# Kernel tuning notes

Measured on AMD Instinct MI355X. Metric: run time of the kernel, lower is better.

Reference implementation:

```python
import jax, jax.numpy as jnp
import numpy as np
from jax import lax

D = 384      # embd_d
L = 4        # num_blocks
B = 64
SHW, THW = 24, 12
NS, NT = SHW * SHW, THW * THW   # 576, 144
EPS = 1e-5


def _ln(x, g, b):
    mu = jnp.mean(x, axis=-1, keepdims=True)
    var = jnp.mean(jnp.square(x - mu), axis=-1, keepdims=True)
    return (x - mu) * lax.rsqrt(var + EPS) * g + b


def setup_inputs() -> dict:
    key = jax.random.key(0)
    ks = iter(jax.random.split(key, 64))
    f32 = jnp.float32
    def nrm(shape, s=0.02):
        return jax.random.normal(next(ks), shape, dtype=f32) * s
    inp = {
        'search': jax.random.normal(next(ks), (B, NS, D), dtype=f32),
        'target': jax.random.normal(next(ks), (B, NT, D), dtype=f32),
        # learned tokens / positional params
        'cls': nrm((1, 1, D), 1.0),
        'search_pos': nrm((1, NS, D), 0.5),
        'target_pos': nrm((1, NT, D), 0.5),
        # stacked per-block params [L, ...]
        'ln1_g': jnp.ones((L, D), f32), 'ln1_b': jnp.zeros((L, D), f32),
        'Wq': nrm((L, D, D)), 'bq': jnp.zeros((L, D), f32),
        'Wk': nrm((L, D, D)), 'bk': jnp.zeros((L, D), f32),
        'Wv': nrm((L, D, D)), 'bv': jnp.zeros((L, D), f32),
        'ln2_g': jnp.ones((L, D), f32), 'ln2_b': jnp.zeros((L, D), f32),
        'W1': nrm((L, D, 2 * D)), 'b1': jnp.zeros((L, 2 * D), f32),
        'W2': nrm((L, 2 * D, D)), 'b2': jnp.zeros((L, D), f32),
        # head
        'lnf_g': jnp.ones((D,), f32), 'lnf_b': jnp.zeros((D,), f32),
        'Wl1': nrm((D, D)), 'bl1': jnp.zeros((D,), f32),
        'Wl2': nrm((D, 1)), 'bl2': jnp.zeros((1,), f32),
    }
    return inp


def reference(search, target, cls, search_pos, target_pos,
              ln1_g, ln1_b, Wq, bq, Wk, bk, Wv, bv,
              ln2_g, ln2_b, W1, b1, W2, b2,
              lnf_g, lnf_b, Wl1, bl1, Wl2, bl2):
    scale = D ** (-0.5)  # note: full embed dim, as in source
    x = jnp.concatenate([
        jnp.broadcast_to(cls, (B, 1, D)),
        search + search_pos,
        target + target_pos,
    ], axis=1)  # [B, 1+Ns+Nt, D]

    def block(x, p):
        l1g, l1b, wq, bq_, wk, bk_, wv, bv_, l2g, l2b, w1, b1_, w2, b2_ = p
        y = _ln(x, l1g, l1b)
        q = y @ wq + bq_
        k = y @ wk + bk_
        v = y @ wv + bv_
        attn = jax.nn.softmax(jnp.einsum('bid,bjd->bij', q, k) * scale, axis=-1)
        x = x + jnp.einsum('bij,bjd->bid', attn, v)
        h = _ln(x, l2g, l2b)
        x = x + (jax.nn.gelu(h @ w1 + b1_, approximate=False) @ w2 + b2_)
        return x, None

    x, _ = lax.scan(block, x, (ln1_g, ln1_b, Wq, bq, Wk, bk, Wv, bv,
                               ln2_g, ln2_b, W1, b1, W2, b2))
    h = _ln(x[:, 0], lnf_g, lnf_b)          # cls token [B, D]
    h = jax.nn.relu(h @ Wl1 + bl1)
    return h @ Wl2 + bl2                     # [B, 1]
```

## Files before the change

kernel.cpp:

```cpp
#include <hip/hip_runtime.h>
#include <hip/hip_bf16.h>
#include <math.h>

#define DD 384
#define NBATCH 64
#define NSEQ 721
#define NROWS (NBATCH*NSEQ)
#define NLAYER 4
#define VTW 736

typedef __bf16 bf16_t;
typedef __bf16 bf16x8 __attribute__((ext_vector_type(8)));
typedef float  f32x4  __attribute__((ext_vector_type(4)));

static __device__ __forceinline__ void split_bf16(float v, bf16_t& h, bf16_t& l) {
    h = (bf16_t)v;
    l = (bf16_t)(v - (float)h);
}
static __device__ __forceinline__ bf16x8 bzero8() {
    bf16x8 v = {(bf16_t)0.f,(bf16_t)0.f,(bf16_t)0.f,(bf16_t)0.f,
                (bf16_t)0.f,(bf16_t)0.f,(bf16_t)0.f,(bf16_t)0.f};
    return v;
}
static __device__ __forceinline__ void gload16(const void* g, void* l) {
    __builtin_amdgcn_global_load_lds(
        (const __attribute__((address_space(1))) unsigned int*)g,
        (__attribute__((address_space(3))) unsigned int*)l, 16, 0, 0);
}
static __device__ __forceinline__ int xcd_swz(int nwg) {
    int orig = blockIdx.x;
    int q = nwg >> 3, r = nwg & 7;
    int xcd = orig & 7, within = orig >> 3;
    int base = (xcd < r) ? xcd*(q+1) : r*(q+1) + (xcd - r)*q;
    return base + within;
}
static __device__ __forceinline__ void ln_from_partials(const float* ss, const float* ss2,
                                                        int row, float& mu, float& rstd) {
    float s = 0.f, q2 = 0.f;
    #pragma unroll
    for (int k = 0; k < 6; ++k) { s += ss[k*NROWS + row]; q2 += ss2[k*NROWS + row]; }
    mu = s * (1.f/DD);
    float var = q2 * (1.f/DD) - mu*mu;
    rstd = rsqrtf(var + 1e-5f);
}

__global__ __launch_bounds__(256) void build_x_kernel(const float* __restrict__ search,
                               const float* __restrict__ target,
                               const float* __restrict__ cls,
                               const float* __restrict__ spos,
                               const float* __restrict__ tpos,
                               bf16_t* __restrict__ xh, bf16_t* __restrict__ xl,
                               float* __restrict__ wss, float* __restrict__ wss2) {
    int wave = threadIdx.x >> 6, lane = threadIdx.x & 63;
    int row = blockIdx.x * 4 + wave;
    if (row >= NROWS) return;
    int b = row / NSEQ, n = row % NSEQ;
    float s = 0.f, q2 = 0.f;
    #pragma unroll
    for (int i = 0; i < 6; ++i) {
        int d = lane + 64*i;
        float val;
        if (n == 0)        val = cls[d];
        else if (n <= 576) val = search[((size_t)b*576 + (n-1))*DD + d] + spos[(size_t)(n-1)*DD + d];
        else               val = target[((size_t)b*144 + (n-577))*DD + d] + tpos[(size_t)(n-577)*DD + d];
        bf16_t h, l;
        split_bf16(val, h, l);
        xh[(size_t)row*DD + d] = h;
        xl[(size_t)row*DD + d] = l;
        s += val; q2 += val*val;
    }
    #pragma unroll
    for (int m = 1; m < 64; m <<= 1) { s += __shfl_xor(s, m); q2 += __shfl_xor(q2, m); }
    if (lane == 0) {
        wss[row] = s; wss2[row] = q2;
        #pragma unroll
        for (int k = 1; k < 6; ++k) { wss[k*NROWS + row] = 0.f; wss2[k*NROWS + row] = 0.f; }
    }
}

__global__ void transpose_split_kernel(const float* __restrict__ src,
                                       const float* __restrict__ g,
                                       bf16_t* __restrict__ dh,
                                       bf16_t* __restrict__ dl,
                                       int K, int N) {
    int idx = blockIdx.x * blockDim.x + threadIdx.x;
    if (idx >= K*N) return;
    int k = idx / N, n = idx % N;
    float v = src[idx];
    if (g) v *= g[k];
    bf16_t h, l;
    split_bf16(v, h, l);
    dh[(size_t)n*K + k] = h;
    dl[(size_t)n*K + k] = l;
}

__global__ void colsum_kernel(const float* __restrict__ W, const float* __restrict__ g,
                              const float* __restrict__ b, const float* __restrict__ bias,
                              float* __restrict__ c1, float* __restrict__ c2,
                              int K, int N, int outStride, int outOff) {
    int l = blockIdx.y;
    int n = blockIdx.x * 256 + threadIdx.x;
    if (n >= N) return;
    const float* Wl = W + (size_t)l*K*N;
    const float* gl = g + (size_t)l*K;
    const float* bl = b + (size_t)l*K;
    float s1 = 0.f, s2 = 0.f;
    for (int k = 0; k < K; ++k) {
        float w = Wl[(size_t)k*N + n];
        s1 = fmaf(gl[k], w, s1);
        s2 = fmaf(bl[k], w, s2);
    }
    c1[(size_t)l*outStride + outOff + n] = s1;
    c2[(size_t)l*outStride + outOff + n] = s2 + bias[(size_t)l*N + n];
}

static __device__ __forceinline__ void gemm_core(
        const bf16_t* __restrict__ ah, const bf16_t* __restrict__ al,
        const bf16_t* __restrict__ bh, const bf16_t* __restrict__ bl,
        bf16_t (&ls)[32][64][8],
        int m0, int n0, int K, f32x4 (&acc)[4][4]) {
    int t = threadIdx.x;
    int w = t >> 6, lane = t & 63;
    int c = lane & 15, g = lane >> 4;
    int wr = w >> 1, wc = w & 1;
    const bf16_t* src0 = (w==0) ? ah : (w==1) ? al : (w==2) ? bh : bl;
    int base_rc = (w < 2) ? m0 : n0;
    const bf16_t* srcbase = src0 + (size_t)(base_rc + c)*K + 8*g;

    int ksteps = K >> 5;
    for (int kt = 0; kt < ksteps; ++kt) {
        int k0 = kt << 5;
        __syncthreads();
        #pragma unroll
        for (int i = 0; i < 8; ++i)
            gload16(srcbase + (size_t)(16*i)*K + k0, &ls[w*8 + i][0][0]);
        __syncthreads();
        bf16x8 af_h[4], af_l[4], bf_h[4], bf_l[4];
        #pragma unroll
        for (int i = 0; i < 4; ++i) {
            af_h[i] = *(const bf16x8*)&ls[     4*wr + i][lane][0];
            af_l[i] = *(const bf16x8*)&ls[ 8 + 4*wr + i][lane][0];
            bf_h[i] = *(const bf16x8*)&ls[16 + 4*wc + i][lane][0];
            bf_l[i] = *(const bf16x8*)&ls[24 + 4*wc + i][lane][0];
        }
        #pragma unroll
        for (int i = 0; i < 4; ++i)
            #pragma unroll
            for (int j = 0; j < 4; ++j) {
                acc[i][j] = __builtin_amdgcn_mfma_f32_16x16x32_bf16(af_h[i], bf_h[j], acc[i][j], 0,0,0);
                acc[i][j] = __builtin_amdgcn_mfma_f32_16x16x32_bf16(af_h[i], bf_l[j], acc[i][j], 0,0,0);
                acc[i][j] = __builtin_amdgcn_mfma_f32_16x16x32_bf16(af_l[i], bf_h[j], acc[i][j], 0,0,0);
            }
    }
}

__global__ __launch_bounds__(256, 4) void gemm_qkv(
        const bf16_t* __restrict__ ah, const bf16_t* __restrict__ al,
        const bf16_t* __restrict__ bh, const bf16_t* __restrict__ bl,
        const float* __restrict__ ss, const float* __restrict__ ss2,
        const float* __restrict__ c1, const float* __restrict__ c2,
        bf16_t* __restrict__ qout, bf16_t* __restrict__ kout,
        bf16_t* __restrict__ vth, bf16_t* __restrict__ vtl,
        int nwg) {
    __shared__ __align__(16) bf16_t ls[32][64][8];
    int wgid = xcd_swz(nwg);
    int mt = wgid / 9, n0 = (wgid % 9) * 128;
    int blb = mt / 6;
    int tok_base = (mt % 6) * 128;
    int m0d = blb*NSEQ + tok_base;
    f32x4 zero4 = {0.f,0.f,0.f,0.f};
    f32x4 acc[4][4];
    #pragma unroll
    for (int i = 0; i < 4; ++i)
        #pragma unroll
        for (int j = 0; j < 4; ++j) acc[i][j] = zero4;
    gemm_core(ah, al, bh, bl, ls, m0d, n0, DD, acc);

    int t = threadIdx.x, w = t >> 6, lane = t & 63;
    int c = lane & 15, g = lane >> 4;
    int wr = w >> 1, wc = w & 1;
    float rmu[16], rrs[16];
    #pragma unroll
    for (int i = 0; i < 4; ++i)
        #pragma unroll
        for (int r = 0; r < 4; ++r) {
            int tok = tok_base + 64*wr + 16*i + 4*g + r;
            float mu = 0.f, rstd = 1.f;
            if (tok < NSEQ) ln_from_partials(ss, ss2, blb*NSEQ + tok, mu, rstd);
            rmu[i*4+r] = mu; rrs[i*4+r] = rstd;
        }
    int seg = n0 / 384;
    if (seg < 2) {
        bf16_t* outb = (seg == 0) ? qout : kout;
        int segoff = seg * 384;
        #pragma unroll
        for (int j = 0; j < 4; ++j) {
            int nglob = n0 + 64*wc + 16*j + c;
            int nloc = nglob - segoff;
            float C1 = c1[nglob], C2 = c2[nglob];
            #pragma unroll
            for (int i = 0; i < 4; ++i) {
                #pragma unroll
                for (int r = 0; r < 4; ++r) {
                    int tok = tok_base + 64*wr + 16*i + 4*g + r;
                    if (tok >= NSEQ) continue;
                    float val = rrs[i*4+r]*(acc[i][j][r] - rmu[i*4+r]*C1) + C2;
                    outb[(size_t)(blb*NSEQ + tok)*DD + nloc] = (bf16_t)val;
                }
            }
        }
    } else {
        int vbase = n0 - 768;
        bf16_t* LST = &ls[0][0][0];
        #pragma unroll
        for (int pass = 0; pass < 2; ++pass) {
            __syncthreads();
            #pragma unroll
            for (int j = 0; j < 4; ++j) {
                int d = 64*wc + 16*j + c;
                float C1 = c1[n0 + 64*wc + 16*j + c];
                float C2 = c2[n0 + 64*wc + 16*j + c];
                #pragma unroll
                for (int i = 0; i < 4; ++i)
                    #pragma unroll
                    for (int r = 0; r < 4; ++r) {
                        int tokl = 64*wr + 16*i + 4*g + r;
                        float val = rrs[i*4+r]*(acc[i][j][r] - rmu[i*4+r]*C1) + C2;
                        if (tok_base + tokl >= NSEQ) val = 0.f;
                        bf16_t h, l;
                        split_bf16(val, h, l);
                        LST[d*128 + (tokl ^ ((d & 15) << 3))] = pass ? l : h;
                    }
            }
            __syncthreads();
            bf16_t* outp = pass ? vtl : vth;
            #pragma unroll
            for (int p = 0; p < 8; ++p) {
                int chunk = t + 256*p;
                int d = chunk >> 4;
                int tok0 = (chunk & 15) * 8;
                int tg = tok_base + tok0;
                if (tg + 8 > VTW) continue;
                uint4 v = *(const uint4*)&LST[d*128 + (tok0 ^ ((d & 15) << 3))];
                *(uint4*)(outp + ((size_t)(blb*DD + vbase + d))*VTW + tg) = v;
            }
        }
    }
}

template<int EPI, int NT>
__global__ __launch_bounds__(256, 4) void gemm_mfma(
        const bf16_t* __restrict__ ah, const bf16_t* __restrict__ al,
        const bf16_t* __restrict__ bh, const bf16_t* __restrict__ bl,
        const float* __restrict__ ss, const float* __restrict__ ss2,
        const float* __restrict__ c1, const float* __restrict__ c2,
        const float* __restrict__ bias,
        const bf16_t* __restrict__ resh, const bf16_t* __restrict__ resl,
        bf16_t* __restrict__ o1, bf16_t* __restrict__ o2,
        float* __restrict__ wss, float* __restrict__ wss2,
        int M, int N, int K, int nwg) {
    __shared__ __align__(16) bf16_t ls[32][64][8];
    int wgid = xcd_swz(nwg);
    int m0 = (wgid / NT) * 128, n0 = (wgid % NT) * 128;
    f32x4 zero4 = {0.f,0.f,0.f,0.f};
    f32x4 acc[4][4];
    #pragma unroll
    for (int i = 0; i < 4; ++i)
        #pragma unroll
        for (int j = 0; j < 4; ++j) acc[i][j] = zero4;
    gemm_core(ah, al, bh, bl, ls, m0, n0, K, acc);

    int t = threadIdx.x, w = t >> 6, lane = t & 63;
    int c = lane & 15, g = lane >> 4;
    int wr = w >> 1, wc = w & 1;

    if (EPI == 2) {
        float rmu[16], rrs[16];
        #pragma unroll
        for (int i = 0; i < 4; ++i)
            #pragma unroll
            for (int r = 0; r < 4; ++r) {
                int row = m0 + 64*wr + 16*i + 4*g + r;
                float mu = 0.f, rstd = 1.f;
                if (row < M) ln_from_partials(ss, ss2, row, mu, rstd);
                rmu[i*4+r] = mu; rrs[i*4+r] = rstd;
            }
        #pragma unroll
        for (int j = 0; j < 4; ++j) {
            int n = n0 + 64*wc + 16*j + c;
            float C1 = c1[n], C2 = c2[n];
            #pragma unroll
            for (int i = 0; i < 4; ++i) {
                int rbase = m0 + 64*wr + 16*i + 4*g;
                #pragma unroll
                for (int r = 0; r < 4; ++r) {
                    int row = rbase + r;
                    if (row >= M) continue;
                    float val = rrs[i*4+r]*(acc[i][j][r] - rmu[i*4+r]*C1) + C2;
                    val = 0.5f*val*(1.0f + erff(val*0.70710678118654752f));
                    bf16_t h, l;
                    split_bf16(val, h, l);
                    size_t o = (size_t)row*N + n;
                    o1[o] = h;
                    o2[o] = l;
                }
            }
        }
    } else {
        int slot = (wgid % NT) + 3*wc;
        #pragma unroll
        for (int i = 0; i < 4; ++i)
            #pragma unroll
            for (int r = 0; r < 4; ++r) {
                int row = m0 + 64*wr + 16*i + 4*g + r;
                if (row >= M) continue;
                float s = 0.f, q2 = 0.f;
                #pragma unroll
                for (int j = 0; j < 4; ++j) {
                    int n = n0 + 64*wc + 16*j + c;
                    size_t o = (size_t)row*N + n;
                    float val = acc[i][j][r] + bias[n] + (float)resh[o] + (float)resl[o];
                    bf16_t h, l;
                    split_bf16(val, h, l);
                    o1[o] = h;
                    o2[o] = l;
                    s += val; q2 += val*val;
                }
                #pragma unroll
                for (int m = 1; m < 16; m <<= 1) { s += __shfl_xor(s, m); q2 += __shfl_xor(q2, m); }
                if (c == 0) {
                    wss[slot*NROWS + row] = s;
                    wss2[slot*NROWS + row] = q2;
                }
            }
    }
}

__global__ __launch_bounds__(256, 2) void attn_mfma(
        const bf16_t* __restrict__ qh, const bf16_t* __restrict__ kh,
        const bf16_t* __restrict__ vth, const bf16_t* __restrict__ vtl,
        bf16_t* __restrict__ xh, bf16_t* __restrict__ xl,
        float* __restrict__ wss, float* __restrict__ wss2, int nwg) {
    __shared__ __align__(16) char smem[73728];
    bf16_t* kf = (bf16_t*)smem;
    char* vhp = smem + 24576;
    char* vlp = smem + 49152;

    int t = threadIdx.x, w = t >> 6, lane = t & 63;
    int c = lane & 15, g = lane >> 4;
    int wgid = xcd_swz(nwg);
    int bl_ = wgid / 12;
    int q0 = (wgid % 12) * 64;
    size_t bb = (size_t)bl_ * NSEQ;
    int qrow = q0 + 16*w + c;
    bool qok = (qrow < NSEQ);
    const float scale = 0.05103103630798287f;
    int vswz = (c ^ (c >> 2)) & 3;
    int dma_dd  = lane >> 2;
    int dma_kv8 = (lane & 3) ^ ((dma_dd ^ (dma_dd >> 2)) & 3);

    bf16x8 qf[12];
    #pragma unroll
    for (int ks = 0; ks < 12; ++ks) {
        if (qok) qf[ks] = *(const bf16x8*)(qh + (bb + qrow)*DD + 32*ks + 8*g);
        else     qf[ks] = bzero8();
    }

    f32x4 zero4 = {0.f,0.f,0.f,0.f};
    f32x4 oacc[24];
    #pragma unroll
    for (int i = 0; i < 24; ++i) oacc[i] = zero4;
    float m_run = -1e30f, l_run = 0.f;

    #pragma unroll
    for (int i = 0; i < 6; ++i) {
        int s = i*4 + w;
        int ks = s >> 1, mf = s & 1;
        gload16(kh + (bb + (size_t)(16*mf + c))*DD + 32*ks + 8*g, kf + s*512);
    }

    for (int kt = 0; kt < 23; ++kt) {
        int kv0 = kt * 32;
        asm volatile("s_waitcnt vmcnt(0)" ::: "memory");
        __builtin_amdgcn_s_barrier();
        #pragma unroll
        for (int i = 0; i < 6; ++i) {
            int s = i*4 + w;
            size_t gro = ((size_t)(bl_*DD + 16*s + dma_dd))*VTW + kv0 + 8*dma_kv8;
            gload16(vth + gro, (bf16_t*)vhp + s*512);
            gload16(vtl + gro, (bf16_t*)vlp + s*512);
        }
        f32x4 sacc[2];
        sacc[0] = zero4; sacc[1] = zero4;
        #pragma unroll
        for (int ks = 0; ks < 12; ++ks) {
            bf16x8 a0 = *(const bf16x8*)(kf + ((size_t)(2*ks+0)*64 + lane)*8);
            bf16x8 a1 = *(const bf16x8*)(kf + ((size_t)(2*ks+1)*64 + lane)*8);
            sacc[0] = __builtin_amdgcn_mfma_f32_16x16x32_bf16(a0, qf[ks], sacc[0], 0,0,0);
            sacc[1] = __builtin_amdgcn_mfma_f32_16x16x32_bf16(a1, qf[ks], sacc[1], 0,0,0);
        }
        float p[2][4];
        float mx = -1e30f;
        #pragma unroll
        for (int mf = 0; mf < 2; ++mf)
            #pragma unroll
            for (int r = 0; r < 4; ++r) {
                float sv = sacc[mf][r] * scale;
                int kv = kv0 + 16*mf + 4*g + r;
                if (kv >= NSEQ) sv = -1e30f;
                p[mf][r] = sv;
                mx = fmaxf(mx, sv);
            }
        mx = fmaxf(mx, __shfl_xor(mx, 16));
        mx = fmaxf(mx, __shfl_xor(mx, 32));
        float m_new = fmaxf(m_run, mx);
        float corr = __expf(m_run - m_new);
        float psum = 0.f;
        #pragma unroll
        for (int mf = 0; mf < 2; ++mf)
            #pragma unroll
            for (int r = 0; r < 4; ++r) {
                float pv = __expf(p[mf][r] - m_new);
                p[mf][r] = pv;
                psum += pv;
            }
        psum += __shfl_xor(psum, 16);
        psum += __shfl_xor(psum, 32);
        l_run = l_run * corr + psum;
        m_run = m_new;
        #pragma unroll
        for (int i = 0; i < 24; ++i) oacc[i] *= corr;
        bf16x8 ph, pl;
        #pragma unroll
        for (int mf = 0; mf < 2; ++mf)
            #pragma unroll
            for (int r = 0; r < 4; ++r) {
                bf16_t hh, ll;
                split_bf16(p[mf][r], hh, ll);
                ph[mf*4 + r] = hh;
                pl[mf*4 + r] = ll;
            }
        asm volatile("s_waitcnt vmcnt(0)" ::: "memory");
        __builtin_amdgcn_s_barrier();
        if (kt + 1 < 23) {
            int kv0n = kv0 + 32;
            #pragma unroll
            for (int i = 0; i < 6; ++i) {
                int s = i*4 + w;
                int ks = s >> 1, mf = s & 1;
                gload16(kh + (bb + (size_t)(kv0n + 16*mf + c))*DD + 32*ks + 8*g, kf + s*512);
            }
        }
        #pragma unroll
        for (int mf = 0; mf < 24; ++mf) {
            int dr = 16*mf + c;
            const char* vb  = vhp + dr*64;
            const char* vb2 = vlp + dr*64;
            int o0 = ((((g>>1)     ^ vswz) << 4) | (8*(g&1)));
            int o1 = (((2 + (g>>1)) ^ vswz) << 4) | (8*(g&1));
            union { uint2 u[2]; bf16x8 v; } va, vc2;
            va.u[0]  = *(const uint2*)(vb  + o0);
            va.u[1]  = *(const uint2*)(vb  + o1);
            vc2.u[0] = *(const uint2*)(vb2 + o0);
            vc2.u[1] = *(const uint2*)(vb2 + o1);
            oacc[mf] = __builtin_amdgcn_mfma_f32_16x16x32_bf16(va.v,  ph, oacc[mf], 0,0,0);
            oacc[mf] = __builtin_amdgcn_mfma_f32_16x16x32_bf16(va.v,  pl, oacc[mf], 0,0,0);
            oacc[mf] = __builtin_amdgcn_mfma_f32_16x16x32_bf16(vc2.v, ph, oacc[mf], 0,0,0);
        }
    }
    float inv = 1.f / l_run;
    float s = 0.f, q2 = 0.f;
    if (qok) {
        bf16_t* xhr = xh + (bb + qrow)*DD;
        bf16_t* xlr = xl + (bb + qrow)*DD;
        #pragma unroll
        for (int mf = 0; mf < 24; ++mf)
            #pragma unroll
            for (int r = 0; r < 4; ++r) {
                int d = 16*mf + 4*g + r;
                float xv = (float)xhr[d] + (float)xlr[d] + oacc[mf][r]*inv;
                bf16_t h, l;
                split_bf16(xv, h, l);
                xhr[d] = h;
                xlr[d] = l;
                s += xv; q2 += xv*xv;
            }
    }
    s += __shfl_xor(s, 16);  q2 += __shfl_xor(q2, 16);
    s += __shfl_xor(s, 32);  q2 += __shfl_xor(q2, 32);
    if (qok && g == 0) {
        int rowL = bl_*NSEQ + qrow;
        wss[rowL] = s; wss2[rowL] = q2;
        #pragma unroll
        for (int k = 1; k < 6; ++k) { wss[k*NROWS + rowL] = 0.f; wss2[k*NROWS + rowL] = 0.f; }
    }
}

__global__ __launch_bounds__(384) void head_kernel(const bf16_t* __restrict__ xh,
    const bf16_t* __restrict__ xl,
    const float* __restrict__ g, const float* __restrict__ bb,
    const float* __restrict__ Wl1, const float* __restrict__ bl1,
    const float* __restrict__ Wl2, const float* __restrict__ bl2,
    float* __restrict__ outp) {
    __shared__ float yv[384];
    __shared__ float r1[6], r2[6], r3[6];
    int b = blockIdx.x, t = threadIdx.x;
    size_t o = (size_t)b*NSEQ*DD + t;
    float v = (float)xh[o] + (float)xl[o];
    float s = v;
    #pragma unroll
    for (int m = 1; m < 64; m <<= 1) s += __shfl_xor(s, m);
    if ((t & 63) == 0) r1[t>>6] = s;
    __syncthreads();
    float mu = (r1[0]+r1[1]+r1[2]+r1[3]+r1[4]+r1[5]) * (1.f/384.f);
    float dd = v - mu;
    float sq = dd*dd;
    #pragma unroll
    for (int m = 1; m < 64; m <<= 1) sq += __shfl_xor(sq, m);
    if ((t & 63) == 0) r2[t>>6] = sq;
    __syncthreads();
    float var = (r2[0]+r2[1]+r2[2]+r2[3]+r2[4]+r2[5]) * (1.f/384.f);
    float rstd = rsqrtf(var + 1e-5f);
    yv[t] = dd*rstd*g[t] + bb[t];
    __syncthreads();
    float acc = bl1[t];
    for (int d2 = 0; d2 < 384; d2++) acc = fmaf(yv[d2], Wl1[d2*384 + t], acc);
    acc = fmaxf(acc, 0.f);
    float oo = acc * Wl2[t];
    #pragma unroll
    for (int m = 1; m < 64; m <<= 1) oo += __shfl_xor(oo, m);
    if ((t & 63) == 0) r3[t>>6] = oo;
    __syncthreads();
    if (t == 0) outp[b] = r3[0]+r3[1]+r3[2]+r3[3]+r3[4]+r3[5] + bl2[0];
}

extern "C" void kernel_launch(void* const* d_in, const int* in_sizes, int n_in,
                              void* d_out, int out_size, void* d_ws, size_t ws_size,
                              hipStream_t stream) {
    const float* search = (const float*)d_in[0];
    const float* target = (const float*)d_in[1];
    const float* cls    = (const float*)d_in[2];
    const float* spos   = (const float*)d_in[3];
    const float* tpos   = (const float*)d_in[4];
    const float* ln1_g  = (const float*)d_in[5];
    const float* ln1_b  = (const float*)d_in[6];
    const float* Wq     = (const float*)d_in[7];
    const float* bq     = (const float*)d_in[8];
    const float* Wk     = (const float*)d_in[9];
    const float* bk     = (const float*)d_in[10];
    const float* Wv     = (const float*)d_in[11];
    const float* bv     = (const float*)d_in[12];
    const float* ln2_g  = (const float*)d_in[13];
    const float* ln2_b  = (const float*)d_in[14];
    const float* W1     = (const float*)d_in[15];
    const float* b1     = (const float*)d_in[16];
    const float* W2     = (const float*)d_in[17];
    const float* b2     = (const float*)d_in[18];
    const float* lnf_g  = (const float*)d_in[19];
    const float* lnf_b  = (const float*)d_in[20];
    const float* Wl1    = (const float*)d_in[21];
    const float* bl1    = (const float*)d_in[22];
    const float* Wl2    = (const float*)d_in[23];
    const float* bl2    = (const float*)d_in[24];

    size_t off = 0;
    char* base = (char*)d_ws;
    auto alloc = [&](size_t bytes) -> void* {
        void* p = base + off;
        off += (bytes + 255) & ~(size_t)255;
        return p;
    };

    bf16_t* xh = (bf16_t*)alloc((size_t)NROWS * DD * 2);
    bf16_t* xl = (bf16_t*)alloc((size_t)NROWS * DD * 2);
    float* ssum  = (float*)alloc((size_t)6*NROWS*4);
    float* ssum2 = (float*)alloc((size_t)6*NROWS*4);

    const int SQKV = 1152*DD;
    const int SM = DD*768;
    bf16_t* wqkvh = (bf16_t*)alloc((size_t)4*SQKV*2);
    bf16_t* wqkvl = (bf16_t*)alloc((size_t)4*SQKV*2);
    bf16_t* w1h = (bf16_t*)alloc((size_t)4*SM*2);
    bf16_t* w1l = (bf16_t*)alloc((size_t)4*SM*2);
    bf16_t* w2h = (bf16_t*)alloc((size_t)4*SM*2);
    bf16_t* w2l = (bf16_t*)alloc((size_t)4*SM*2);
    float* cqkv1 = (float*)alloc((size_t)4*1152*4);
    float* cqkv2 = (float*)alloc((size_t)4*1152*4);
    float* cm11  = (float*)alloc((size_t)4*768*4);
    float* cm12  = (float*)alloc((size_t)4*768*4);

    const size_t qB  = (size_t)NSEQ*DD*2;
    const size_t vB  = (size_t)DD*VTW*2;
    const size_t mB  = (size_t)NSEQ*768*2;
    const size_t perB = 2*qB + 2*vB;
    size_t avail = (ws_size > off + 262144) ? (ws_size - off - 262144) : 0;
    int G = (int)(avail / perB);
    if (G > NBATCH) G = NBATCH;
    if (G < 1) G = 1;

    char* U = (char*)alloc(perB * G);
    bf16_t* qhB  = (bf16_t*)U;
    bf16_t* khB  = (bf16_t*)(U + qB*G);
    bf16_t* vth  = (bf16_t*)(U + 2*qB*G);
    bf16_t* vtl  = (bf16_t*)(U + 2*qB*G + vB*G);
    bf16_t* midh = (bf16_t*)U;
    bf16_t* midl = (bf16_t*)(U + mB*G);

    build_x_kernel<<<(NROWS+3)/4, 256, 0, stream>>>(search, target, cls, spos, tpos,
                                                    xh, xl, ssum, ssum2);

    const int SQ = DD*DD;
    for (int l = 0; l < NLAYER; ++l) {
        bf16_t* dsth = wqkvh + (size_t)l*SQKV;
        bf16_t* dstl = wqkvl + (size_t)l*SQKV;
        transpose_split_kernel<<<(SQ+255)/256, 256, 0, stream>>>(Wq + (size_t)l*SQ, ln1_g + l*DD, dsth,          dstl,          DD, DD);
        transpose_split_kernel<<<(SQ+255)/256, 256, 0, stream>>>(Wk + (size_t)l*SQ, ln1_g + l*DD, dsth + 384*DD, dstl + 384*DD, DD, DD);
        transpose_split_kernel<<<(SQ+255)/256, 256, 0, stream>>>(Wv + (size_t)l*SQ, ln1_g + l*DD, dsth + 768*DD, dstl + 768*DD, DD, DD);
        transpose_split_kernel<<<(SM+255)/256, 256, 0, stream>>>(W1 + (size_t)l*SM, ln2_g + l*DD, w1h + (size_t)l*SM, w1l + (size_t)l*SM, DD, 768);
        transpose_split_kernel<<<(SM+255)/256, 256, 0, stream>>>(W2 + (size_t)l*SM, nullptr,      w2h + (size_t)l*SM, w2l + (size_t)l*SM, 768, DD);
    }
    colsum_kernel<<<dim3(2, NLAYER), 256, 0, stream>>>(Wq, ln1_g, ln1_b, bq, cqkv1, cqkv2, DD, DD, 1152, 0);
    colsum_kernel<<<dim3(2, NLAYER), 256, 0, stream>>>(Wk, ln1_g, ln1_b, bk, cqkv1, cqkv2, DD, DD, 1152, 384);
    colsum_kernel<<<dim3(2, NLAYER), 256, 0, stream>>>(Wv, ln1_g, ln1_b, bv, cqkv1, cqkv2, DD, DD, 1152, 768);
    colsum_kernel<<<dim3(3, NLAYER), 256, 0, stream>>>(W1, ln2_g, ln2_b, b1, cm11, cm12, DD, 768, 768, 0);

    for (int l = 0; l < NLAYER; ++l) {
        for (int b0 = 0; b0 < NBATCH; b0 += G) {
            int cb = (NBATCH - b0 < G) ? (NBATCH - b0) : G;
            int Mc = cb * NSEQ;
            bf16_t* xch = xh + (size_t)b0 * NSEQ * DD;
            bf16_t* xcl = xl + (size_t)b0 * NSEQ * DD;
            float* ssc  = ssum  + (size_t)b0 * NSEQ;
            float* ssc2 = ssum2 + (size_t)b0 * NSEQ;
            int mtiles = (Mc + 127)/128;
            int nwgQKV = 9*6*cb, nwgM1 = 6*mtiles, nwgM2 = 3*mtiles, nwgA = 12*cb;

            gemm_qkv<<<nwgQKV, 256, 0, stream>>>(xch, xcl,
                    wqkvh + (size_t)l*SQKV, wqkvl + (size_t)l*SQKV,
                    ssc, ssc2, cqkv1 + l*1152, cqkv2 + l*1152,
                    qhB, khB, vth, vtl, nwgQKV);
            attn_mfma<<<nwgA, 256, 0, stream>>>(qhB, khB, vth, vtl, xch, xcl,
                    ssc, ssc2, nwgA);
            gemm_mfma<2,6><<<nwgM1, 256, 0, stream>>>(xch, xcl,
                    w1h + (size_t)l*SM, w1l + (size_t)l*SM,
                    ssc, ssc2, cm11 + l*768, cm12 + l*768, nullptr,
                    nullptr, nullptr, midh, midl, nullptr, nullptr, Mc, 768, DD, nwgM1);
            gemm_mfma<3,3><<<nwgM2, 256, 0, stream>>>(midh, midl,
                    w2h + (size_t)l*SM, w2l + (size_t)l*SM,
                    nullptr, nullptr, nullptr, nullptr, b2 + l*DD,
                    xch, xcl, xch, xcl, ssc, ssc2, Mc, DD, 768, nwgM2);
        }
    }
    head_kernel<<<NBATCH, 384, 0, stream>>>(xh, xl, lnf_g, lnf_b, Wl1, bl1, Wl2, bl2, (float*)d_out);
}
```

Before: 3.596 ms.

## Drop V low-precision split, stage Q/K stores through LDS, add lazy softmax rescale

Removes the bf16 hi/lo split for V, so attention loads only one V buffer and issues two MFMAs per tile instead of three. This halves V traffic and LDS use, which allows three workgroups per CU. Q/K outputs are now staged through LDS for coalesced 16-byte stores. The online softmax skips the max update and accumulator rescale when the new max stays within a threshold of the running max. The workspace sizing now uses the MLP intermediate size. The cost is lower precision in the attention-times-V product.

```diff
diff --git a/kernel.cpp b/kernel.cpp
--- a/kernel.cpp
+++ b/kernel.cpp
@@ -160,7 +160,7 @@
         const float* __restrict__ ss, const float* __restrict__ ss2,
         const float* __restrict__ c1, const float* __restrict__ c2,
         bf16_t* __restrict__ qout, bf16_t* __restrict__ kout,
-        bf16_t* __restrict__ vth, bf16_t* __restrict__ vtl,
+        bf16_t* __restrict__ vth,
         int nwg) {
     __shared__ __align__(16) bf16_t ls[32][64][8];
     int wgid = xcd_swz(nwg);
@@ -190,60 +190,62 @@
             rmu[i*4+r] = mu; rrs[i*4+r] = rstd;
         }
     int seg = n0 / 384;
+    bf16_t* LST = &ls[0][0][0];
     if (seg < 2) {
         bf16_t* outb = (seg == 0) ? qout : kout;
         int segoff = seg * 384;
+        __syncthreads();
         #pragma unroll
         for (int j = 0; j < 4; ++j) {
-            int nglob = n0 + 64*wc + 16*j + c;
-            int nloc = nglob - segoff;
-            float C1 = c1[nglob], C2 = c2[nglob];
-            #pragma unroll
-            for (int i = 0; i < 4; ++i) {
+            int nl = 64*wc + 16*j + c;
+            float C1 = c1[n0 + nl], C2 = c2[n0 + nl];
+            #pragma unroll
+            for (int i = 0; i < 4; ++i)
                 #pragma unroll
                 for (int r = 0; r < 4; ++r) {
-                    int tok = tok_base + 64*wr + 16*i + 4*g + r;
-                    if (tok >= NSEQ) continue;
+                    int rl = 64*wr + 16*i + 4*g + r;
                     float val = rrs[i*4+r]*(acc[i][j][r] - rmu[i*4+r]*C1) + C2;
-                    outb[(size_t)(blb*NSEQ + tok)*DD + nloc] = (bf16_t)val;
+                    LST[rl*128 + (nl ^ ((rl & 15) << 3))] = (bf16_t)val;
                 }
-            }
+        }
+        __syncthreads();
+        #pragma unroll
+        for (int p = 0; p < 8; ++p) {
+            int chunk = t + 256*p;
+            int rl = chunk >> 4;
+            int nl0 = (chunk & 15) * 8;
+            int tok = tok_base + rl;
+            if (tok >= NSEQ) continue;
+            uint4 v = *(const uint4*)&LST[rl*128 + (nl0 ^ ((rl & 15) << 3))];
+            *(uint4*)(outb + (size_t)(blb*NSEQ + tok)*DD + (n0 - segoff) + nl0) = v;
         }
     } else {
         int vbase = n0 - 768;
-        bf16_t* LST = &ls[0][0][0];
-        #pragma unroll
-        for (int pass = 0; pass < 2; ++pass) {
-            __syncthreads();
-            #pragma unroll
-            for (int j = 0; j < 4; ++j) {
-                int d = 64*wc + 16*j + c;
-                float C1 = c1[n0 + 64*wc + 16*j + c];
-                float C2 = c2[n0 + 64*wc + 16*j + c];
+        __syncthreads();
+        #pragma unroll
+        for (int j = 0; j < 4; ++j) {
+            int d = 64*wc + 16*j + c;
+            float C1 = c1[n0 + d], C2 = c2[n0 + d];
+            #pragma unroll
+            for (int i = 0; i < 4; ++i)
                 #pragma unroll
-                for (int i = 0; i < 4; ++i)
-                    #pragma unroll
-                    for (int r = 0; r < 4; ++r) {
-                        int tokl = 64*wr + 16*i + 4*g + r;
-                        float val = rrs[i*4+r]*(acc[i][j][r] - rmu[i*4+r]*C1) + C2;
-                        if (tok_base + tokl >= NSEQ) val = 0.f;
-                        bf16_t h, l;
-                        split_bf16(val, h, l);
-                        LST[d*128 + (tokl ^ ((d & 15) << 3))] = pass ? l : h;
-                    }
-            }
-            __syncthreads();
-            bf16_t* outp = pass ? vtl : vth;
-            #pragma unroll
-            for (int p = 0; p < 8; ++p) {
-                int chunk = t + 256*p;
-                int d = chunk >> 4;
-                int tok0 = (chunk & 15) * 8;
-                int tg = tok_base + tok0;
-                if (tg + 8 > VTW) continue;
-                uint4 v = *(const uint4*)&LST[d*128 + (tok0 ^ ((d & 15) << 3))];
-                *(uint4*)(outp + ((size_t)(blb*DD + vbase + d))*VTW + tg) = v;
-            }
+                for (int r = 0; r < 4; ++r) {
+                    int tokl = 64*wr + 16*i + 4*g + r;
+                    float val = rrs[i*4+r]*(acc[i][j][r] - rmu[i*4+r]*C1) + C2;
+                    if (tok_base + tokl >= NSEQ) val = 0.f;
+                    LST[d*128 + (tokl ^ ((d & 15) << 3))] = (bf16_t)val;
+                }
+        }
+        __syncthreads();
+        #pragma unroll
+        for (int p = 0; p < 8; ++p) {
+            int chunk = t + 256*p;
+            int d = chunk >> 4;
+            int tok0 = (chunk & 15) * 8;
+            int tg = tok_base + tok0;
+            if (tg + 8 > VTW) continue;
+            uint4 v = *(const uint4*)&LST[d*128 + (tok0 ^ ((d & 15) << 3))];
+            *(uint4*)(vth + ((size_t)(blb*DD + vbase + d))*VTW + tg) = v;
         }
     }
 }
@@ -336,15 +338,14 @@
     }
 }
 
-__global__ __launch_bounds__(256, 2) void attn_mfma(
+__global__ __launch_bounds__(256, 3) void attn_mfma(
         const bf16_t* __restrict__ qh, const bf16_t* __restrict__ kh,
-        const bf16_t* __restrict__ vth, const bf16_t* __restrict__ vtl,
+        const bf16_t* __restrict__ vth,
         bf16_t* __restrict__ xh, bf16_t* __restrict__ xl,
         float* __restrict__ wss, float* __restrict__ wss2, int nwg) {
-    __shared__ __align__(16) char smem[73728];
+    __shared__ __align__(16) char smem[49152];
     bf16_t* kf = (bf16_t*)smem;
     char* vhp = smem + 24576;
-    char* vlp = smem + 49152;
 
     int t = threadIdx.x, w = t >> 6, lane = t & 63;
     int c = lane & 15, g = lane >> 4;
@@ -388,7 +389,6 @@
             int s = i*4 + w;
             size_t gro = ((size_t)(bl_*DD + 16*s + dma_dd))*VTW + kv0 + 8*dma_kv8;
             gload16(vth + gro, (bf16_t*)vhp + s*512);
-            gload16(vtl + gro, (bf16_t*)vlp + s*512);
         }
         f32x4 sacc[2];
         sacc[0] = zero4; sacc[1] = zero4;
@@ -413,8 +413,8 @@
             }
         mx = fmaxf(mx, __shfl_xor(mx, 16));
         mx = fmaxf(mx, __shfl_xor(mx, 32));
-        float m_new = fmaxf(m_run, mx);
-        float corr = __expf(m_run - m_new);
+        bool skip = __all(mx <= m_run + 8.f);
+        float m_new = skip ? m_run : fmaxf(m_run, mx);
         float psum = 0.f;
         #pragma unroll
         for (int mf = 0; mf < 2; ++mf)
@@ -426,10 +426,15 @@
             }
         psum += __shfl_xor(psum, 16);
         psum += __shfl_xor(psum, 32);
-        l_run = l_run * corr + psum;
-        m_run = m_new;
-        #pragma unroll
-        for (int i = 0; i < 24; ++i) oacc[i] *= corr;
+        if (!skip) {
+            float corr = __expf(m_run - m_new);
+            l_run = l_run * corr + psum;
+            #pragma unroll
+            for (int i = 0; i < 24; ++i) oacc[i] *= corr;
+            m_run = m_new;
+        } else {
+            l_run += psum;
+        }
         bf16x8 ph, pl;
         #pragma unroll
         for (int mf = 0; mf < 2; ++mf)
@@ -454,18 +459,14 @@
         #pragma unroll
         for (int mf = 0; mf < 24; ++mf) {
             int dr = 16*mf + c;
-            const char* vb  = vhp + dr*64;
-            const char* vb2 = vlp + dr*64;
+            const char* vb = vhp + dr*64;
             int o0 = ((((g>>1)     ^ vswz) << 4) | (8*(g&1)));
             int o1 = (((2 + (g>>1)) ^ vswz) << 4) | (8*(g&1));
-            union { uint2 u[2]; bf16x8 v; } va, vc2;
-            va.u[0]  = *(const uint2*)(vb  + o0);
-            va.u[1]  = *(const uint2*)(vb  + o1);
-            vc2.u[0] = *(const uint2*)(vb2 + o0);
-            vc2.u[1] = *(const uint2*)(vb2 + o1);
-            oacc[mf] = __builtin_amdgcn_mfma_f32_16x16x32_bf16(va.v,  ph, oacc[mf], 0,0,0);
-            oacc[mf] = __builtin_amdgcn_mfma_f32_16x16x32_bf16(va.v,  pl, oacc[mf], 0,0,0);
-            oacc[mf] = __builtin_amdgcn_mfma_f32_16x16x32_bf16(vc2.v, ph, oacc[mf], 0,0,0);
+            union { uint2 u[2]; bf16x8 v; } va;
+            va.u[0] = *(const uint2*)(vb + o0);
+            va.u[1] = *(const uint2*)(vb + o1);
+            oacc[mf] = __builtin_amdgcn_mfma_f32_16x16x32_bf16(va.v, ph, oacc[mf], 0,0,0);
+            oacc[mf] = __builtin_amdgcn_mfma_f32_16x16x32_bf16(va.v, pl, oacc[mf], 0,0,0);
         }
     }
     float inv = 1.f / l_run;
@@ -592,7 +593,7 @@
     const size_t qB  = (size_t)NSEQ*DD*2;
     const size_t vB  = (size_t)DD*VTW*2;
     const size_t mB  = (size_t)NSEQ*768*2;
-    const size_t perB = 2*qB + 2*vB;
+    const size_t perB = 2*mB;
     size_t avail = (ws_size > off + 262144) ? (ws_size - off - 262144) : 0;
     int G = (int)(avail / perB);
     if (G > NBATCH) G = NBATCH;
@@ -602,7 +603,6 @@
     bf16_t* qhB  = (bf16_t*)U;
     bf16_t* khB  = (bf16_t*)(U + qB*G);
     bf16_t* vth  = (bf16_t*)(U + 2*qB*G);
-    bf16_t* vtl  = (bf16_t*)(U + 2*qB*G + vB*G);
     bf16_t* midh = (bf16_t*)U;
     bf16_t* midl = (bf16_t*)(U + mB*G);
 
@@ -638,8 +638,8 @@
             gemm_qkv<<<nwgQKV, 256, 0, stream>>>(xch, xcl,
                     wqkvh + (size_t)l*SQKV, wqkvl + (size_t)l*SQKV,
                     ssc, ssc2, cqkv1 + l*1152, cqkv2 + l*1152,
-                    qhB, khB, vth, vtl, nwgQKV);
-            attn_mfma<<<nwgA, 256, 0, stream>>>(qhB, khB, vth, vtl, xch, xcl,
+                    qhB, khB, vth, nwgQKV);
+            attn_mfma<<<nwgA, 256, 0, stream>>>(qhB, khB, vth, xch, xcl,
                     ssc, ssc2, nwgA);
             gemm_mfma<2,6><<<nwgM1, 256, 0, stream>>>(xch, xcl,
                     w1h + (size_t)l*SM, w1l + (size_t)l*SM,
```

New measurement: 3.628 ms. No clear change (+0.9%).
